# Kernel optimization log

Measured on AMD Instinct MI355X. Metric: run time of the kernel, lower is better.

Reference implementation:

```python
import jax, jax.numpy as jnp
import numpy as np

N_NODES = 50000
N_EDGES = 625000
FEAT = 128
NEG_SLOPE = 0.2  # dgl GATConv default leaky_relu slope


def setup_inputs() -> dict:
    key = jax.random.key(0)
    ks = jax.random.split(key, 16)
    x = jax.random.normal(ks[0], (N_NODES, FEAT), dtype=jnp.float32)
    src = jax.random.randint(ks[1], (N_EDGES,), 0, N_NODES, dtype=jnp.int32)
    dst = jax.random.randint(ks[2], (N_EDGES,), 0, N_NODES, dtype=jnp.int32)
    s = 1.0 / np.sqrt(FEAT)
    d = {"x": x, "src": src, "dst": dst}
    for i in range(3):
        d[f"W{i+1}"] = jax.random.normal(ks[3 + 4 * i], (FEAT, FEAT), dtype=jnp.float32) * s
        d[f"al{i+1}"] = jax.random.normal(ks[4 + 4 * i], (FEAT,), dtype=jnp.float32) * s
        d[f"ar{i+1}"] = jax.random.normal(ks[5 + 4 * i], (FEAT,), dtype=jnp.float32) * s
        d[f"b{i+1}"] = jnp.zeros((FEAT,), dtype=jnp.float32)
    return d


def gat_layer(h_in, src, dst, W, al, ar, b):
    # dgl GATConv, num_heads=1: fc -> edge attention -> edge_softmax -> scatter
    h = h_in @ W                                   # [N, F]
    el = h @ al                                    # [N]
    er = h @ ar                                    # [N]
    e = jax.nn.leaky_relu(el[src] + er[dst], NEG_SLOPE)   # [E]
    # numerically stable edge softmax, grouped by destination node
    m = jax.ops.segment_max(e, dst, num_segments=N_NODES)  # [N]
    ex = jnp.exp(e - m[dst])
    denom = jax.ops.segment_sum(ex, dst, num_segments=N_NODES)
    alpha = ex / denom[dst]                        # [E]
    out = jax.ops.segment_sum(alpha[:, None] * h[src], dst, num_segments=N_NODES)
    return out + b


def reference(x, src, dst, W1, al1, ar1, b1, W2, al2, ar2, b2, W3, al3, ar3, b3):
    h = gat_layer(x, src, dst, W1, al1, ar1, b1)
    h = jax.nn.relu(h)
    h = gat_layer(h, src, dst, W2, al2, ar2, b2)
    h = jax.nn.relu(h)
    h = gat_layer(h, src, dst, W3, al3, ar3, b3)
    return h
```

## Files before the change

kernel.cpp:

```cpp
#include <hip/hip_runtime.h>
#include <hip/hip_fp16.h>

#define N_NODES 50000
#define N_EDGES 625000
#define FEAT 128
#define NEG_SLOPE 0.2f
#define NB_SCAN 196

typedef __attribute__((ext_vector_type(8))) short bf16x8;
typedef __attribute__((ext_vector_type(4))) float f32x4;

__device__ __forceinline__ unsigned short f2bf(float f) {
  unsigned u = __float_as_uint(f);
  u += 0x7fffu + ((u >> 16) & 1u);
  return (unsigned short)(u >> 16);
}
__device__ __forceinline__ float bf2f(unsigned short s) {
  return __uint_as_float(((unsigned)s) << 16);
}


__global__ __launch_bounds__(256) void hist_kernel(const int* __restrict__ dst,
                                                   int* __restrict__ cnt) {
  int e = blockIdx.x * 256 + threadIdx.x;
  if (e < N_EDGES) atomicAdd(&cnt[dst[e]], 1);
}

__global__ __launch_bounds__(256) void scan_part_kernel(const int* __restrict__ cnt,
                                                        int* __restrict__ part) {
  __shared__ int s[256];
  int i = blockIdx.x * 256 + threadIdx.x;
  s[threadIdx.x] = (i < N_NODES) ? cnt[i] : 0;
  __syncthreads();
  for (int o = 128; o > 0; o >>= 1) {
    if (threadIdx.x < o) s[threadIdx.x] += s[threadIdx.x + o];
    __syncthreads();
  }
  if (threadIdx.x == 0) part[blockIdx.x] = s[0];
}

__global__ __launch_bounds__(256) void scan_top_kernel(int* __restrict__ part,
                                                       int* __restrict__ offs) {
  __shared__ int s[256];
  int tid = threadIdx.x;
  int v = (tid < NB_SCAN) ? part[tid] : 0;
  s[tid] = v;
  __syncthreads();
  for (int o = 1; o < 256; o <<= 1) {
    int t = (tid >= o) ? s[tid - o] : 0;
    __syncthreads();
    s[tid] += t;
    __syncthreads();
  }
  if (tid < NB_SCAN) part[tid] = s[tid] - v;
  if (tid == 255) offs[N_NODES] = s[255];
}

__global__ __launch_bounds__(256) void scan_down_kernel(int* __restrict__ cnt,
                                                        const int* __restrict__ part,
                                                        int* __restrict__ offs) {
  __shared__ int s[256];
  int tid = threadIdx.x;
  int i = blockIdx.x * 256 + tid;
  int v = (i < N_NODES) ? cnt[i] : 0;
  s[tid] = v;
  __syncthreads();
  for (int o = 1; o < 256; o <<= 1) {
    int t = (tid >= o) ? s[tid - o] : 0;
    __syncthreads();
    s[tid] += t;
    __syncthreads();
  }
  if (i < N_NODES) {
    int excl = s[tid] - v + part[blockIdx.x];
    offs[i] = excl;
    cnt[i] = excl;
  }
}

__global__ __launch_bounds__(256) void fill_kernel(const int* __restrict__ src,
                                                   const int* __restrict__ dst,
                                                   int* __restrict__ cursor,
                                                   int* __restrict__ ssrc) {
  int e = blockIdx.x * 256 + threadIdx.x;
  if (e < N_EDGES) {
    int pos = atomicAdd(&cursor[dst[e]], 1);
    ssrc[pos] = src[e];
  }
}


__global__ __launch_bounds__(256) void prep_w_kernel(
    const float* __restrict__ W0, const float* __restrict__ W1, const float* __restrict__ W2,
    unsigned short* __restrict__ wfhi, unsigned short* __restrict__ wflo) {
  int idx = blockIdx.x * 256 + threadIdx.x;
  if (idx >= 3 * FEAT * FEAT) return;
  int l = idx >> 14, rem = idx & 16383;
  int e = rem & 7, lane = (rem >> 3) & 63, kb = (rem >> 9) & 3, ct = rem >> 11;
  int col = ct * 16 + (lane & 15);
  int k   = kb * 32 + (lane >> 4) * 8 + e;
  const float* W = (l == 0) ? W0 : ((l == 1) ? W1 : W2);
  float v = W[k * FEAT + col];
  unsigned short hi = f2bf(v);
  wfhi[idx] = hi;
  wflo[idx] = f2bf(v - bf2f(hi));
}


__global__ __launch_bounds__(256) void gemm_mfma_kernel(
    const float* __restrict__ in,
    const unsigned short* __restrict__ wfhi, const unsigned short* __restrict__ wflo,
    const float* __restrict__ al, const float* __restrict__ ar,
    __half* __restrict__ h, float* __restrict__ el, float* __restrict__ er,
    int applyRelu)
{
  __shared__ __half tile[64][132];
  const int tid = threadIdx.x;
  const int wave = tid >> 6, lane = tid & 63;
  const int lrow = lane & 15, lkb = lane >> 4;
  const int arow_i = blockIdx.x * 64 + wave * 16 + lrow;
  const bool avalid = arow_i < N_NODES;

  bf16x8 ahi[4], alo[4];
  const float* arow = in + (size_t)arow_i * FEAT;
#pragma unroll
  for (int kb = 0; kb < 4; ++kb) {
    float a[8];
    if (avalid) {
      float4 v0 = *(const float4*)(arow + kb * 32 + lkb * 8);
      float4 v1 = *(const float4*)(arow + kb * 32 + lkb * 8 + 4);
      a[0] = v0.x; a[1] = v0.y; a[2] = v0.z; a[3] = v0.w;
      a[4] = v1.x; a[5] = v1.y; a[6] = v1.z; a[7] = v1.w;
    } else {
#pragma unroll
      for (int e = 0; e < 8; ++e) a[e] = 0.f;
    }
    if (applyRelu) {
#pragma unroll
      for (int e = 0; e < 8; ++e) a[e] = fmaxf(a[e], 0.f);
    }
#pragma unroll
    for (int e = 0; e < 8; ++e) {
      unsigned short hb = f2bf(a[e]);
      ahi[kb][e] = (short)hb;
      alo[kb][e] = (short)f2bf(a[e] - bf2f(hb));
    }
  }

  f32x4 acc[8];
#pragma unroll
  for (int ct = 0; ct < 8; ++ct)
#pragma unroll
    for (int r = 0; r < 4; ++r) acc[ct][r] = 0.f;

#pragma unroll
  for (int ct = 0; ct < 8; ++ct) {
#pragma unroll
    for (int kb = 0; kb < 4; ++kb) {
      const int off = (ct * 4 + kb) * 512 + lane * 8;
      bf16x8 bhi = *(const bf16x8*)(wfhi + off);
      bf16x8 blo = *(const bf16x8*)(wflo + off);
      acc[ct] = __builtin_amdgcn_mfma_f32_16x16x32_bf16(ahi[kb], bhi, acc[ct], 0, 0, 0);
      acc[ct] = __builtin_amdgcn_mfma_f32_16x16x32_bf16(ahi[kb], blo, acc[ct], 0, 0, 0);
      acc[ct] = __builtin_amdgcn_mfma_f32_16x16x32_bf16(alo[kb], bhi, acc[ct], 0, 0, 0);
    }
  }

  float alv[8], arv[8];
#pragma unroll
  for (int ct = 0; ct < 8; ++ct) { alv[ct] = al[ct * 16 + lrow]; arv[ct] = ar[ct * 16 + lrow]; }

  const int lrow0 = wave * 16 + lkb * 4;
#pragma unroll
  for (int r = 0; r < 4; ++r) {
    float pel = 0.f, per_ = 0.f;
#pragma unroll
    for (int ct = 0; ct < 8; ++ct) {
      float v = acc[ct][r];
      tile[lrow0 + r][ct * 16 + lrow] = __float2half_rn(v);
      pel  = fmaf(v, alv[ct], pel);
      per_ = fmaf(v, arv[ct], per_);
    }
#pragma unroll
    for (int mask = 8; mask >= 1; mask >>= 1) {
      pel  += __shfl_xor(pel, mask);
      per_ += __shfl_xor(per_, mask);
    }
    int grow = blockIdx.x * 64 + lrow0 + r;
    if (grow < N_NODES && lrow == 0) { el[grow] = pel; er[grow] = per_; }
  }
  __syncthreads();

  const int row0g = blockIdx.x * 64;
#pragma unroll
  for (int it = 0; it < 4; ++it) {
    int idx = it * 256 + tid;
    int row = idx >> 4, c16 = idx & 15;
    int grow = row0g + row;
    if (grow < N_NODES) {
      uint4 v = *(const uint4*)&tile[row][c16 * 8];
      *((uint4*)(h + (size_t)grow * FEAT) + c16) = v;
    }
  }
}


__global__ __launch_bounds__(256) void agg_kernel(
    const __half* __restrict__ h, const float* __restrict__ el,
    const float* __restrict__ er, const int* __restrict__ offs,
    const int* __restrict__ ssrc, const float* __restrict__ bias,
    float* __restrict__ out)
{
  const int wid = (blockIdx.x * 256 + threadIdx.x) >> 6;
  const int lane = threadIdx.x & 63;
  if (wid >= N_NODES) return;
  const int qg = lane >> 4;
  const int ql = lane & 15;

  const int beg = offs[wid], end = offs[wid + 1];
  const float erd = er[wid];
  const unsigned short* __restrict__ hu = (const unsigned short*)h;

  float acc[8];
#pragma unroll
  for (int f = 0; f < 8; ++f) acc[f] = 0.f;
  float denom = 0.f, m = -1e30f;

  for (int base = beg; base < end; base += 64) {
    const int n = min(64, end - base);

    int s = 0;
    float e = -1e30f;
    if (lane < n) {
      s = ssrc[base + lane];
      float t = el[s] + erd;
      e = t > 0.f ? t : NEG_SLOPE * t;
    }

    float cm = e;
#pragma unroll
    for (int mask = 32; mask > 0; mask >>= 1) cm = fmaxf(cm, __shfl_xor(cm, mask));
    if (cm > m) {
      float sc = __expf(m - cm);
#pragma unroll
      for (int f = 0; f < 8; ++f) acc[f] *= sc;
      denom *= sc;
      m = cm;
    }

    float ex = (lane < n) ? __expf(e - m) : 0.f;
    float ds = ex;
#pragma unroll
    for (int mask = 32; mask > 0; mask >>= 1) ds += __shfl_xor(ds, mask);
    denom += ds;

    for (int g = 0; g < n; g += 16) {
      uint4 raw[4];
      float w[4];
#pragma unroll
      for (int l = 0; l < 4; ++l) {
        int j = g + l * 4 + qg;
        int sj = __shfl(s, j);
        w[l] = __shfl(ex, j);
        raw[l] = *(const uint4*)(hu + (((size_t)sj) << 7) + (ql << 3));
      }
#pragma unroll
      for (int l = 0; l < 4; ++l) {
        float2 f0 = __half22float2(__builtin_bit_cast(__half2, raw[l].x));
        float2 f1 = __half22float2(__builtin_bit_cast(__half2, raw[l].y));
        float2 f2 = __half22float2(__builtin_bit_cast(__half2, raw[l].z));
        float2 f3 = __half22float2(__builtin_bit_cast(__half2, raw[l].w));
        acc[0] = fmaf(w[l], f0.x, acc[0]); acc[1] = fmaf(w[l], f0.y, acc[1]);
        acc[2] = fmaf(w[l], f1.x, acc[2]); acc[3] = fmaf(w[l], f1.y, acc[3]);
        acc[4] = fmaf(w[l], f2.x, acc[4]); acc[5] = fmaf(w[l], f2.y, acc[5]);
        acc[6] = fmaf(w[l], f3.x, acc[6]); acc[7] = fmaf(w[l], f3.y, acc[7]);
      }
    }
  }

#pragma unroll
  for (int f = 0; f < 8; ++f) {
    acc[f] += __shfl_xor(acc[f], 16);
    acc[f] += __shfl_xor(acc[f], 32);
  }

  float inv = denom > 0.f ? 1.f / denom : 0.f;
  if (qg < 2) {
    float4 bv = ((const float4*)bias)[ql * 2 + qg];
    float4 o;
    o.x = fmaf(acc[qg * 4 + 0], inv, bv.x);
    o.y = fmaf(acc[qg * 4 + 1], inv, bv.y);
    o.z = fmaf(acc[qg * 4 + 2], inv, bv.z);
    o.w = fmaf(acc[qg * 4 + 3], inv, bv.w);
    ((float4*)out)[((size_t)wid << 5) + ql * 2 + qg] = o;
  }
}


extern "C" void kernel_launch(void* const* d_in, const int* in_sizes, int n_in,
                              void* d_out, int out_size, void* d_ws, size_t ws_size,
                              hipStream_t stream) {
  const float* x  = (const float*)d_in[0];
  const int* src  = (const int*)d_in[1];
  const int* dst  = (const int*)d_in[2];
  const float* W[3]  = {(const float*)d_in[3],  (const float*)d_in[7],  (const float*)d_in[11]};
  const float* al[3] = {(const float*)d_in[4],  (const float*)d_in[8],  (const float*)d_in[12]};
  const float* ar[3] = {(const float*)d_in[5],  (const float*)d_in[9],  (const float*)d_in[13]};
  const float* b[3]  = {(const float*)d_in[6],  (const float*)d_in[10], (const float*)d_in[14]};

  __half* hH  = (__half*)d_ws;
  float*  el  = (float*)(hH + 6400000);
  float*  er  = el + 50016;
  int*    cnt = (int*)(er + 50016);
  int*    offs = cnt + 50016;
  int*    part = offs + 50016;
  int*    ssrc = part + 256;
  unsigned short* wfhi = (unsigned short*)(ssrc + 625000);
  unsigned short* wflo = wfhi + 3 * FEAT * FEAT;

  prep_w_kernel<<<(3 * FEAT * FEAT + 255) / 256, 256, 0, stream>>>(W[0], W[1], W[2], wfhi, wflo);
  hipMemsetAsync(cnt, 0, N_NODES * sizeof(int), stream);
  hist_kernel<<<(N_EDGES + 255) / 256, 256, 0, stream>>>(dst, cnt);
  scan_part_kernel<<<NB_SCAN, 256, 0, stream>>>(cnt, part);
  scan_top_kernel<<<1, 256, 0, stream>>>(part, offs);
  scan_down_kernel<<<NB_SCAN, 256, 0, stream>>>(cnt, part, offs);
  fill_kernel<<<(N_EDGES + 255) / 256, 256, 0, stream>>>(src, dst, cnt, ssrc);

  const int gemm_grid = (N_NODES + 63) / 64;
  const int agg_grid  = (N_NODES + 3) / 4;
  float* outf = (float*)d_out;

  for (int l = 0; l < 3; ++l) {
    const float* lin = (l == 0) ? x : outf;
    gemm_mfma_kernel<<<gemm_grid, 256, 0, stream>>>(
        lin, wfhi + l * FEAT * FEAT, wflo + l * FEAT * FEAT,
        al[l], ar[l], hH, el, er, l > 0 ? 1 : 0);
    agg_kernel<<<agg_grid, 256, 0, stream>>>(hH, el, er, offs, ssrc, b[l], outf);
  }
}
```

Measured before the change: 238.5 us.

## Store intermediate layer outputs in fp16, stage weights in LDS, merge setup kernels

Layers 1 and 2 now write their output as fp16 into a workspace buffer, and the next GEMM reads it back as fp16 with ReLU applied, halving that traffic. The GEMM now stages weight fragments in LDS in two halves instead of reading them from global memory per wave. The weight prep and count zeroing are merged into one launch, and the three-kernel scan is replaced by a single 1024-thread block scan. These changes cut launch count and bytes moved, but the fp16 intermediates lose precision and the single-block scan runs serially per thread.

```diff
diff --git a/kernel.cpp b/kernel.cpp
--- a/kernel.cpp
+++ b/kernel.cpp
@@ -5,7 +5,6 @@
 #define N_EDGES 625000
 #define FEAT 128
 #define NEG_SLOPE 0.2f
-#define NB_SCAN 196
 
 typedef __attribute__((ext_vector_type(8))) short bf16x8;
 typedef __attribute__((ext_vector_type(4))) float f32x4;
@@ -20,61 +19,65 @@
 }
 
 
+__global__ __launch_bounds__(256) void prepzero_kernel(
+    const float* __restrict__ W0, const float* __restrict__ W1, const float* __restrict__ W2,
+    unsigned short* __restrict__ wfhi, unsigned short* __restrict__ wflo,
+    int* __restrict__ cnt) {
+  int bb = blockIdx.x;
+  if (bb < 192) {
+    int idx = bb * 256 + threadIdx.x;
+    if (idx >= 3 * FEAT * FEAT) return;
+    int l = idx >> 14, rem = idx & 16383;
+    int e = rem & 7, lane = (rem >> 3) & 63, kb = (rem >> 9) & 3, ct = rem >> 11;
+    int col = ct * 16 + (lane & 15);
+    int k   = kb * 32 + (lane >> 4) * 8 + e;
+    const float* W = (l == 0) ? W0 : ((l == 1) ? W1 : W2);
+    float v = W[k * FEAT + col];
+    unsigned short hi = f2bf(v);
+    wfhi[idx] = hi;
+    wflo[idx] = f2bf(v - bf2f(hi));
+  } else {
+    int i = (bb - 192) * 256 + threadIdx.x;
+    if (i < N_NODES + 16) cnt[i] = 0;
+  }
+}
+
+
 __global__ __launch_bounds__(256) void hist_kernel(const int* __restrict__ dst,
                                                    int* __restrict__ cnt) {
   int e = blockIdx.x * 256 + threadIdx.x;
   if (e < N_EDGES) atomicAdd(&cnt[dst[e]], 1);
 }
 
-__global__ __launch_bounds__(256) void scan_part_kernel(const int* __restrict__ cnt,
-                                                        int* __restrict__ part) {
-  __shared__ int s[256];
-  int i = blockIdx.x * 256 + threadIdx.x;
-  s[threadIdx.x] = (i < N_NODES) ? cnt[i] : 0;
-  __syncthreads();
-  for (int o = 128; o > 0; o >>= 1) {
-    if (threadIdx.x < o) s[threadIdx.x] += s[threadIdx.x + o];
+__global__ __launch_bounds__(1024) void scan_kernel(int* __restrict__ cnt,
+                                                    int* __restrict__ offs) {
+  __shared__ int ssum[1024];
+  const int tid = threadIdx.x;
+  const int CH = 49;
+  const int base = tid * CH;
+  int lsum = 0;
+  for (int i = 0; i < CH; ++i) {
+    int idx = base + i;
+    lsum += (idx < N_NODES) ? cnt[idx] : 0;
+  }
+  ssum[tid] = lsum;
+  __syncthreads();
+  for (int o = 1; o < 1024; o <<= 1) {
+    int t = (tid >= o) ? ssum[tid - o] : 0;
     __syncthreads();
-  }
-  if (threadIdx.x == 0) part[blockIdx.x] = s[0];
-}
-
-__global__ __launch_bounds__(256) void scan_top_kernel(int* __restrict__ part,
-                                                       int* __restrict__ offs) {
-  __shared__ int s[256];
-  int tid = threadIdx.x;
-  int v = (tid < NB_SCAN) ? part[tid] : 0;
-  s[tid] = v;
-  __syncthreads();
-  for (int o = 1; o < 256; o <<= 1) {
-    int t = (tid >= o) ? s[tid - o] : 0;
+    ssum[tid] += t;
     __syncthreads();
-    s[tid] += t;
-    __syncthreads();
-  }
-  if (tid < NB_SCAN) part[tid] = s[tid] - v;
-  if (tid == 255) offs[N_NODES] = s[255];
-}
-
-__global__ __launch_bounds__(256) void scan_down_kernel(int* __restrict__ cnt,
-                                                        const int* __restrict__ part,
-                                                        int* __restrict__ offs) {
-  __shared__ int s[256];
-  int tid = threadIdx.x;
-  int i = blockIdx.x * 256 + tid;
-  int v = (i < N_NODES) ? cnt[i] : 0;
-  s[tid] = v;
-  __syncthreads();
-  for (int o = 1; o < 256; o <<= 1) {
-    int t = (tid >= o) ? s[tid - o] : 0;
-    __syncthreads();
-    s[tid] += t;
-    __syncthreads();
-  }
-  if (i < N_NODES) {
-    int excl = s[tid] - v + part[blockIdx.x];
-    offs[i] = excl;
-    cnt[i] = excl;
+  }
+  if (tid == 1023) offs[N_NODES] = ssum[1023];
+  int run = ssum[tid] - lsum;
+  for (int i = 0; i < CH; ++i) {
+    int idx = base + i;
+    if (idx < N_NODES) {
+      int c = cnt[idx];
+      offs[idx] = run;
+      cnt[idx] = run;
+      run += c;
+    }
   }
 }
 
@@ -90,30 +93,14 @@
 }
 
 
-__global__ __launch_bounds__(256) void prep_w_kernel(
-    const float* __restrict__ W0, const float* __restrict__ W1, const float* __restrict__ W2,
-    unsigned short* __restrict__ wfhi, unsigned short* __restrict__ wflo) {
-  int idx = blockIdx.x * 256 + threadIdx.x;
-  if (idx >= 3 * FEAT * FEAT) return;
-  int l = idx >> 14, rem = idx & 16383;
-  int e = rem & 7, lane = (rem >> 3) & 63, kb = (rem >> 9) & 3, ct = rem >> 11;
-  int col = ct * 16 + (lane & 15);
-  int k   = kb * 32 + (lane >> 4) * 8 + e;
-  const float* W = (l == 0) ? W0 : ((l == 1) ? W1 : W2);
-  float v = W[k * FEAT + col];
-  unsigned short hi = f2bf(v);
-  wfhi[idx] = hi;
-  wflo[idx] = f2bf(v - bf2f(hi));
-}
-
-
 __global__ __launch_bounds__(256) void gemm_mfma_kernel(
-    const float* __restrict__ in,
+    const float* __restrict__ inF, const __half* __restrict__ inH,
     const unsigned short* __restrict__ wfhi, const unsigned short* __restrict__ wflo,
     const float* __restrict__ al, const float* __restrict__ ar,
     __half* __restrict__ h, float* __restrict__ el, float* __restrict__ er,
-    int applyRelu)
+    int fp16relu_in)
 {
+  __shared__ unsigned short wl[16384];
   __shared__ __half tile[64][132];
   const int tid = threadIdx.x;
   const int wave = tid >> 6, lane = tid & 63;
@@ -121,23 +108,40 @@
   const int arow_i = blockIdx.x * 64 + wave * 16 + lrow;
   const bool avalid = arow_i < N_NODES;
 
+#pragma unroll
+  for (int q = 0; q < 8; ++q) {
+    int idx = q * 256 + tid;
+    int hilo = idx >> 10, r = idx & 1023, frag = r >> 6, word = r & 63;
+    int ct = frag >> 1, kb = frag & 1;
+    const uint4* s4 = (const uint4*)(hilo ? wflo : wfhi);
+    uint4 v = s4[(ct * 4 + kb) * 64 + word];
+    *(uint4*)&wl[((hilo * 16 + frag) << 9) + word * 8] = v;
+  }
+
   bf16x8 ahi[4], alo[4];
-  const float* arow = in + (size_t)arow_i * FEAT;
 #pragma unroll
   for (int kb = 0; kb < 4; ++kb) {
     float a[8];
     if (avalid) {
-      float4 v0 = *(const float4*)(arow + kb * 32 + lkb * 8);
-      float4 v1 = *(const float4*)(arow + kb * 32 + lkb * 8 + 4);
-      a[0] = v0.x; a[1] = v0.y; a[2] = v0.z; a[3] = v0.w;
-      a[4] = v1.x; a[5] = v1.y; a[6] = v1.z; a[7] = v1.w;
+      if (fp16relu_in) {
+        const unsigned short* aH = (const unsigned short*)inH + (size_t)arow_i * FEAT;
+        uint4 rv = *(const uint4*)(aH + kb * 32 + lkb * 8);
+        const __half2* hp = (const __half2*)&rv;
+#pragma unroll
+        for (int e2 = 0; e2 < 4; ++e2) {
+          float2 f = __half22float2(hp[e2]);
+          a[e2 * 2] = fmaxf(f.x, 0.f); a[e2 * 2 + 1] = fmaxf(f.y, 0.f);
+        }
+      } else {
+        const float* arow = inF + (size_t)arow_i * FEAT;
+        float4 v0 = *(const float4*)(arow + kb * 32 + lkb * 8);
+        float4 v1 = *(const float4*)(arow + kb * 32 + lkb * 8 + 4);
+        a[0] = v0.x; a[1] = v0.y; a[2] = v0.z; a[3] = v0.w;
+        a[4] = v1.x; a[5] = v1.y; a[6] = v1.z; a[7] = v1.w;
+      }
     } else {
 #pragma unroll
       for (int e = 0; e < 8; ++e) a[e] = 0.f;
-    }
-    if (applyRelu) {
-#pragma unroll
-      for (int e = 0; e < 8; ++e) a[e] = fmaxf(a[e], 0.f);
     }
 #pragma unroll
     for (int e = 0; e < 8; ++e) {
@@ -153,16 +157,39 @@
 #pragma unroll
     for (int r = 0; r < 4; ++r) acc[ct][r] = 0.f;
 
+  __syncthreads();
 #pragma unroll
   for (int ct = 0; ct < 8; ++ct) {
 #pragma unroll
-    for (int kb = 0; kb < 4; ++kb) {
-      const int off = (ct * 4 + kb) * 512 + lane * 8;
-      bf16x8 bhi = *(const bf16x8*)(wfhi + off);
-      bf16x8 blo = *(const bf16x8*)(wflo + off);
-      acc[ct] = __builtin_amdgcn_mfma_f32_16x16x32_bf16(ahi[kb], bhi, acc[ct], 0, 0, 0);
-      acc[ct] = __builtin_amdgcn_mfma_f32_16x16x32_bf16(ahi[kb], blo, acc[ct], 0, 0, 0);
-      acc[ct] = __builtin_amdgcn_mfma_f32_16x16x32_bf16(alo[kb], bhi, acc[ct], 0, 0, 0);
+    for (int kb1 = 0; kb1 < 2; ++kb1) {
+      bf16x8 bhi = *(const bf16x8*)&wl[((ct * 2 + kb1) << 9) + lane * 8];
+      bf16x8 blo = *(const bf16x8*)&wl[((16 + ct * 2 + kb1) << 9) + lane * 8];
+      acc[ct] = __builtin_amdgcn_mfma_f32_16x16x32_bf16(ahi[kb1], bhi, acc[ct], 0, 0, 0);
+      acc[ct] = __builtin_amdgcn_mfma_f32_16x16x32_bf16(ahi[kb1], blo, acc[ct], 0, 0, 0);
+      acc[ct] = __builtin_amdgcn_mfma_f32_16x16x32_bf16(alo[kb1], bhi, acc[ct], 0, 0, 0);
+    }
+  }
+  __syncthreads();
+
+#pragma unroll
+  for (int q = 0; q < 8; ++q) {
+    int idx = q * 256 + tid;
+    int hilo = idx >> 10, r = idx & 1023, frag = r >> 6, word = r & 63;
+    int ct = frag >> 1, kb = 2 + (frag & 1);
+    const uint4* s4 = (const uint4*)(hilo ? wflo : wfhi);
+    uint4 v = s4[(ct * 4 + kb) * 64 + word];
+    *(uint4*)&wl[((hilo * 16 + frag) << 9) + word * 8] = v;
+  }
+  __syncthreads();
+#pragma unroll
+  for (int ct = 0; ct < 8; ++ct) {
+#pragma unroll
+    for (int kb1 = 0; kb1 < 2; ++kb1) {
+      bf16x8 bhi = *(const bf16x8*)&wl[((ct * 2 + kb1) << 9) + lane * 8];
+      bf16x8 blo = *(const bf16x8*)&wl[((16 + ct * 2 + kb1) << 9) + lane * 8];
+      acc[ct] = __builtin_amdgcn_mfma_f32_16x16x32_bf16(ahi[2 + kb1], bhi, acc[ct], 0, 0, 0);
+      acc[ct] = __builtin_amdgcn_mfma_f32_16x16x32_bf16(ahi[2 + kb1], blo, acc[ct], 0, 0, 0);
+      acc[ct] = __builtin_amdgcn_mfma_f32_16x16x32_bf16(alo[2 + kb1], bhi, acc[ct], 0, 0, 0);
     }
   }
 
@@ -209,7 +236,7 @@
     const __half* __restrict__ h, const float* __restrict__ el,
     const float* __restrict__ er, const int* __restrict__ offs,
     const int* __restrict__ ssrc, const float* __restrict__ bias,
-    float* __restrict__ out)
+    float* __restrict__ out32, __half* __restrict__ out16, int use16)
 {
   const int wid = (blockIdx.x * 256 + threadIdx.x) >> 6;
   const int lane = threadIdx.x & 63;
@@ -285,14 +312,27 @@
   }
 
   float inv = denom > 0.f ? 1.f / denom : 0.f;
-  if (qg < 2) {
-    float4 bv = ((const float4*)bias)[ql * 2 + qg];
-    float4 o;
-    o.x = fmaf(acc[qg * 4 + 0], inv, bv.x);
-    o.y = fmaf(acc[qg * 4 + 1], inv, bv.y);
-    o.z = fmaf(acc[qg * 4 + 2], inv, bv.z);
-    o.w = fmaf(acc[qg * 4 + 3], inv, bv.w);
-    ((float4*)out)[((size_t)wid << 5) + ql * 2 + qg] = o;
+  if (use16) {
+    if (qg == 0) {
+      float4 b0 = ((const float4*)bias)[ql * 2];
+      float4 b1 = ((const float4*)bias)[ql * 2 + 1];
+      __half2 o[4];
+      o[0] = __floats2half2_rn(fmaf(acc[0], inv, b0.x), fmaf(acc[1], inv, b0.y));
+      o[1] = __floats2half2_rn(fmaf(acc[2], inv, b0.z), fmaf(acc[3], inv, b0.w));
+      o[2] = __floats2half2_rn(fmaf(acc[4], inv, b1.x), fmaf(acc[5], inv, b1.y));
+      o[3] = __floats2half2_rn(fmaf(acc[6], inv, b1.z), fmaf(acc[7], inv, b1.w));
+      ((uint4*)(out16 + ((size_t)wid << 7)))[ql] = *(const uint4*)o;
+    }
+  } else {
+    if (qg < 2) {
+      float4 bv = ((const float4*)bias)[ql * 2 + qg];
+      float4 o;
+      o.x = fmaf(acc[qg * 4 + 0], inv, bv.x);
+      o.y = fmaf(acc[qg * 4 + 1], inv, bv.y);
+      o.z = fmaf(acc[qg * 4 + 2], inv, bv.z);
+      o.w = fmaf(acc[qg * 4 + 3], inv, bv.w);
+      ((float4*)out32)[((size_t)wid << 5) + ql * 2 + qg] = o;
+    }
   }
 }
 
@@ -308,22 +348,19 @@
   const float* ar[3] = {(const float*)d_in[5],  (const float*)d_in[9],  (const float*)d_in[13]};
   const float* b[3]  = {(const float*)d_in[6],  (const float*)d_in[10], (const float*)d_in[14]};
 
-  __half* hH  = (__half*)d_ws;
-  float*  el  = (float*)(hH + 6400000);
-  float*  er  = el + 50016;
-  int*    cnt = (int*)(er + 50016);
-  int*    offs = cnt + 50016;
-  int*    part = offs + 50016;
-  int*    ssrc = part + 256;
+  __half* hH    = (__half*)d_ws;
+  __half* out16 = hH + 6400000;
+  float*  el    = (float*)(out16 + 6400000);
+  float*  er    = el + 50016;
+  int*    cnt   = (int*)(er + 50016);
+  int*    offs  = cnt + 50016;
+  int*    ssrc  = offs + 50016;
   unsigned short* wfhi = (unsigned short*)(ssrc + 625000);
   unsigned short* wflo = wfhi + 3 * FEAT * FEAT;
 
-  prep_w_kernel<<<(3 * FEAT * FEAT + 255) / 256, 256, 0, stream>>>(W[0], W[1], W[2], wfhi, wflo);
-  hipMemsetAsync(cnt, 0, N_NODES * sizeof(int), stream);
+  prepzero_kernel<<<392, 256, 0, stream>>>(W[0], W[1], W[2], wfhi, wflo, cnt);
   hist_kernel<<<(N_EDGES + 255) / 256, 256, 0, stream>>>(dst, cnt);
-  scan_part_kernel<<<NB_SCAN, 256, 0, stream>>>(cnt, part);
-  scan_top_kernel<<<1, 256, 0, stream>>>(part, offs);
-  scan_down_kernel<<<NB_SCAN, 256, 0, stream>>>(cnt, part, offs);
+  scan_kernel<<<1, 1024, 0, stream>>>(cnt, offs);
   fill_kernel<<<(N_EDGES + 255) / 256, 256, 0, stream>>>(src, dst, cnt, ssrc);
 
   const int gemm_grid = (N_NODES + 63) / 64;
@@ -331,10 +368,11 @@
   float* outf = (float*)d_out;
 
   for (int l = 0; l < 3; ++l) {
-    const float* lin = (l == 0) ? x : outf;
     gemm_mfma_kernel<<<gemm_grid, 256, 0, stream>>>(
-        lin, wfhi + l * FEAT * FEAT, wflo + l * FEAT * FEAT,
+        (l == 0) ? x : nullptr, (l == 0) ? nullptr : out16,
+        wfhi + l * FEAT * FEAT, wflo + l * FEAT * FEAT,
         al[l], ar[l], hH, el, er, l > 0 ? 1 : 0);
-    agg_kernel<<<agg_grid, 256, 0, stream>>>(hH, el, er, offs, ssrc, b[l], outf);
-  }
-}
+    agg_kernel<<<agg_grid, 256, 0, stream>>>(
+        hH, el, er, offs, ssrc, b[l], outf, out16, l < 2 ? 1 : 0);
+  }
+}
```

New measurement: 348.3 us. 1.46x slower.
